# Kernel tuning notes

Measured on AMD Instinct MI355X. Metric: run time of the kernel, lower is better.

Reference implementation:

```python
import jax, jax.numpy as jnp
import numpy as np

T, B, L, D = 4, 2, 2048, 4096

def setup_inputs() -> dict:
    key = jax.random.key(0)
    x = jax.random.normal(key, (T, B, L, D), dtype=jnp.float32)
    return {"x": x}

def reference(x):
    # X_t = sum_{s<=t} x_s ; Y_t = silu(X_t) ; out_t = Y_t - Y_{t-1}, Y_{-1}=0
    X = jnp.cumsum(x, axis=0)            # (T,B,L,D)
    Y = jax.nn.silu(X)                   # act_fn default "silu"
    Y_prev = jnp.concatenate([jnp.zeros_like(Y[:1]), Y[:-1]], axis=0)
    return Y - Y_prev
```

## Files before the change

### kernel.cpp

```cpp
#include <hip/hip_runtime.h>
#include <math.h>


#define T_STEPS 4

typedef float v4f __attribute__((ext_vector_type(4)));

__device__ __forceinline__ v4f silu4(v4f X) {
    v4f r;
    r.x = X.x * __builtin_amdgcn_rcpf(1.0f + __expf(-X.x));
    r.y = X.y * __builtin_amdgcn_rcpf(1.0f + __expf(-X.y));
    r.z = X.z * __builtin_amdgcn_rcpf(1.0f + __expf(-X.z));
    r.w = X.w * __builtin_amdgcn_rcpf(1.0f + __expf(-X.w));
    return r;
}

__global__ __launch_bounds__(256) void ActSWL_kernel(const v4f* __restrict__ xv,
                                                     v4f* __restrict__ ov,
                                                     unsigned n_vec) {
    unsigned i = blockIdx.x * 256u + threadIdx.x;
    if (i >= n_vec) return;

    v4f v0 = __builtin_nontemporal_load(xv + i);
    v4f v1 = __builtin_nontemporal_load(xv + i + n_vec);
    v4f v2 = __builtin_nontemporal_load(xv + i + 2u * n_vec);
    v4f v3 = __builtin_nontemporal_load(xv + i + 3u * n_vec);

    v4f X  = v0;
    v4f y0 = silu4(X);
    X += v1;
    v4f y1 = silu4(X);
    X += v2;
    v4f y2 = silu4(X);
    X += v3;
    v4f y3 = silu4(X);

    __builtin_nontemporal_store(y0,      ov + i);
    __builtin_nontemporal_store(y1 - y0, ov + i + n_vec);
    __builtin_nontemporal_store(y2 - y1, ov + i + 2u * n_vec);
    __builtin_nontemporal_store(y3 - y2, ov + i + 3u * n_vec);
}

extern "C" void kernel_launch(void* const* d_in, const int* in_sizes, int n_in,
                              void* d_out, int out_size, void* d_ws, size_t ws_size,
                              hipStream_t stream) {
    const v4f* xv = (const v4f*)d_in[0];
    v4f* ov       = (v4f*)d_out;

    const long long n_total = (long long)in_sizes[0];
    const unsigned n_vec    = (unsigned)(n_total / T_STEPS / 4);

    const int block = 256;
    const unsigned grid = (n_vec + block - 1) / block;

    ActSWL_kernel<<<dim3(grid), dim3(block), 0, stream>>>(xv, ov, n_vec);
}
```

Before: 429.6 us.

## Use grid-stride loop with software-prefetched next iteration loads

Caps the grid at 2048 blocks and turns the kernel into a grid-stride loop. Each iteration issues the four loads for the next chunk before computing and storing the current one, so memory latency overlaps with compute. This cuts block launch overhead but uses more registers and gives less parallelism per wave.

```diff
diff --git a/kernel.cpp b/kernel.cpp
--- a/kernel.cpp
+++ b/kernel.cpp
@@ -18,27 +18,47 @@
 __global__ __launch_bounds__(256) void ActSWL_kernel(const v4f* __restrict__ xv,
                                                      v4f* __restrict__ ov,
                                                      unsigned n_vec) {
-    unsigned i = blockIdx.x * 256u + threadIdx.x;
-    if (i >= n_vec) return;
+    const unsigned stride = gridDim.x * 256u;
+    unsigned idx = blockIdx.x * 256u + threadIdx.x;
+    if (idx >= n_vec) return;
 
-    v4f v0 = __builtin_nontemporal_load(xv + i);
-    v4f v1 = __builtin_nontemporal_load(xv + i + n_vec);
-    v4f v2 = __builtin_nontemporal_load(xv + i + 2u * n_vec);
-    v4f v3 = __builtin_nontemporal_load(xv + i + 3u * n_vec);
+    const unsigned n1 = n_vec, n2 = 2u * n_vec, n3 = 3u * n_vec;
 
-    v4f X  = v0;
-    v4f y0 = silu4(X);
-    X += v1;
-    v4f y1 = silu4(X);
-    X += v2;
-    v4f y2 = silu4(X);
-    X += v3;
-    v4f y3 = silu4(X);
+    v4f a0 = __builtin_nontemporal_load(xv + idx);
+    v4f a1 = __builtin_nontemporal_load(xv + idx + n1);
+    v4f a2 = __builtin_nontemporal_load(xv + idx + n2);
+    v4f a3 = __builtin_nontemporal_load(xv + idx + n3);
 
-    __builtin_nontemporal_store(y0,      ov + i);
-    __builtin_nontemporal_store(y1 - y0, ov + i + n_vec);
-    __builtin_nontemporal_store(y2 - y1, ov + i + 2u * n_vec);
-    __builtin_nontemporal_store(y3 - y2, ov + i + 3u * n_vec);
+    for (;;) {
+        const unsigned nxt = idx + stride;
+        const bool more = nxt < n_vec;
+
+        v4f b0, b1, b2, b3;
+        if (more) {
+            b0 = __builtin_nontemporal_load(xv + nxt);
+            b1 = __builtin_nontemporal_load(xv + nxt + n1);
+            b2 = __builtin_nontemporal_load(xv + nxt + n2);
+            b3 = __builtin_nontemporal_load(xv + nxt + n3);
+        }
+
+        v4f X  = a0;
+        v4f y0 = silu4(X);
+        X += a1;
+        v4f y1 = silu4(X);
+        X += a2;
+        v4f y2 = silu4(X);
+        X += a3;
+        v4f y3 = silu4(X);
+
+        __builtin_nontemporal_store(y0,      ov + idx);
+        __builtin_nontemporal_store(y1 - y0, ov + idx + n1);
+        __builtin_nontemporal_store(y2 - y1, ov + idx + n2);
+        __builtin_nontemporal_store(y3 - y2, ov + idx + n3);
+
+        if (!more) break;
+        a0 = b0; a1 = b1; a2 = b2; a3 = b3;
+        idx = nxt;
+    }
 }
 
 extern "C" void kernel_launch(void* const* d_in, const int* in_sizes, int n_in,
@@ -51,7 +71,8 @@
     const unsigned n_vec    = (unsigned)(n_total / T_STEPS / 4);
 
     const int block = 256;
-    const unsigned grid = (n_vec + block - 1) / block;
+    unsigned grid = (n_vec + block - 1) / block;
+    if (grid > 2048u) grid = 2048u;
 
     ActSWL_kernel<<<dim3(grid), dim3(block), 0, stream>>>(xv, ov, n_vec);
 }
```

After: 425.8 us. Within noise of the previous version (-0.9%).
